# Kernel tuning notes

Measured on AMD Instinct MI355X. Metric: run time of the kernel, lower is better.

## Reference

```python
import jax, jax.numpy as jnp
import numpy as np

PATCH = 64      # patch generator patch size
LD = 1.0        # self.ld
WS = 11         # SSIM gaussian window size
SIGMA = 1.5
C1 = 0.01 ** 2
C2 = 0.03 ** 2


def _gauss_window(channels):
    x = jnp.arange(WS, dtype=jnp.float32)
    g = jnp.exp(-((x - WS // 2) ** 2) / (2.0 * SIGMA * SIGMA))
    g = g / g.sum()
    w2 = jnp.outer(g, g)               # (WS, WS), sums to 1
    return jnp.broadcast_to(w2[None, None], (channels, 1, WS, WS))


def _dwconv(x, w, channels):
    # depthwise 'same' conv, padding = WS//2 (matches F.conv2d(..., padding=ws//2, groups=C))
    p = WS // 2
    return jax.lax.conv_general_dilated(
        x, w, window_strides=(1, 1), padding=[(p, p), (p, p)],
        dimension_numbers=("NCHW", "OIHW", "NCHW"), feature_group_count=channels)


def _ssim(img1, img2):
    # img1, img2: (n, C, h, w) -> per-image mean SSIM, shape (n,)
    ch = img1.shape[1]
    w = _gauss_window(ch).astype(img1.dtype)
    mu1 = _dwconv(img1, w, ch)
    mu2 = _dwconv(img2, w, ch)
    mu1_sq, mu2_sq, mu1_mu2 = mu1 * mu1, mu2 * mu2, mu1 * mu2
    sigma1_sq = _dwconv(img1 * img1, w, ch) - mu1_sq
    sigma2_sq = _dwconv(img2 * img2, w, ch) - mu2_sq
    sigma12 = _dwconv(img1 * img2, w, ch) - mu1_mu2
    ssim_map = ((2.0 * mu1_mu2 + C1) * (2.0 * sigma12 + C2)) / (
        (mu1_sq + mu2_sq + C1) * (sigma1_sq + sigma2_sq + C2))
    return jnp.mean(ssim_map, axis=(1, 2, 3))


def _to_patches(x, ps):
    # (B, C, H, W) -> (B, P, C, ps, ps) with P = (H//ps)*(W//ps)
    B, C, H, W = x.shape
    x = x.reshape(B, C, H // ps, ps, W // ps, ps)
    x = x.transpose(0, 2, 4, 1, 3, 5)
    return x.reshape(B, (H // ps) * (W // ps), C, ps, ps)


def setup_inputs() -> dict:
    key = jax.random.key(0)
    ks = jax.random.split(key, 5)
    shp = (32, 3, 512, 512)
    names = ["A", "N", "GT", "G", "BG"]
    return {n: jax.random.uniform(k, shp, dtype=jnp.float32) for n, k in zip(names, ks)}


def reference(A, N, GT, G, BG):
    pA = _to_patches(A, PATCH)
    pN = _to_patches(N, PATCH)
    pGT = _to_patches(GT, PATCH)
    pG = _to_patches(G, PATCH)
    pBG = _to_patches(BG, PATCH)
    B, P, C, h, w = pA.shape
    # batched SSIM over all (B*P) patches (replaces the python double loop)
    ssim_scores = _ssim(pN.reshape(B * P, C, h, w), pGT.reshape(B * P, C, h, w)).reshape(B, P)
    diff = jnp.minimum(LD * (1.0 - ssim_scores), jnp.ones_like(ssim_scores))
    bg_loss = jnp.mean((pBG - pG) ** 2, axis=(2, 3, 4))
    a_loss = jnp.mean((pA - pG) ** 2, axis=(2, 3, 4))
    loss = diff * bg_loss + (1.0 - diff) * a_loss
    return jnp.sum(loss)
```

## Files before the change

kernel.cpp:

```cpp
#include <hip/hip_runtime.h>
#include <math.h>

#define C1C 1e-4f
#define C2C 9e-4f

#define GW0 0.00102838f
#define GW1 0.00759876f
#define GW2 0.03600077f
#define GW3 0.10936069f
#define GW4 0.21300554f
#define GW5 0.26601173f
__device__ __forceinline__ float conv11(const float* w) {
    float a = GW0 * (w[0] + w[10]);
    a = fmaf(GW1, w[1] + w[9], a);
    a = fmaf(GW2, w[2] + w[8], a);
    a = fmaf(GW3, w[3] + w[7], a);
    a = fmaf(GW4, w[4] + w[6], a);
    a = fmaf(GW5, w[5], a);
    return a;
}

#define SROWS 74
#define SSTR  36

__global__ __launch_bounds__(256, 3) void ssim_fused_kernel(
    const float* __restrict__ A,  const float* __restrict__ Nimg,
    const float* __restrict__ GT, const float* __restrict__ G,
    const float* __restrict__ BG,
    float* __restrict__ ssim_sum, float* __restrict__ sa_sum,
    float* __restrict__ sbg_sum)
{
    __shared__ float S0[SROWS][SSTR];
    __shared__ float S1[SROWS][SSTR];
    __shared__ float S2[SROWS][SSTR];
    __shared__ float S3[SROWS][SSTR];
    __shared__ float S4[SROWS][SSTR];

    const int q  = blockIdx.x;
    const int c  = blockIdx.y;
    const int b  = q >> 6;
    const int pp = q & 63;
    const int ph = pp >> 3;
    const int pw = pp & 7;
    const unsigned base = ((unsigned)(b * 3 + c) << 18)
                        + ((unsigned)(ph * 64) << 9)
                        + (unsigned)(pw * 64);
    const int t = threadIdx.x;

    for (int i = t; i < 10 * SSTR; i += 256) {
        const int r  = i / SSTR;
        const int cc = i - r * SSTR;
        const int rr = (r < 5) ? r : 64 + r;
        S0[rr][cc] = 0.f; S1[rr][cc] = 0.f; S2[rr][cc] = 0.f;
        S3[rr][cc] = 0.f; S4[rr][cc] = 0.f;
    }

    const int hr   = t >> 2;
    const int hseg = t & 3;
    const int c0   = hseg << 3;
    const unsigned rowBase = base + ((unsigned)hr << 9);
    const int vcol = t & 31;
    const int vr0  = (t >> 5) << 3;

    float accS = 0.f;

    for (int h = 0; h < 2; ++h) {
        const int g0 = (h << 5) + c0;
        float xs[18], ys[18];
        #pragma unroll
        for (int m = 0; m < 6; ++m) {
            const int cb = g0 - 8 + 4 * m;
            float4 xv = make_float4(0.f, 0.f, 0.f, 0.f);
            float4 yv = make_float4(0.f, 0.f, 0.f, 0.f);
            if (cb >= 0 && cb < 64) {
                xv = *(const float4*)(Nimg + rowBase + cb);
                yv = *(const float4*)(GT   + rowBase + cb);
            }
            #pragma unroll
            for (int u = 0; u < 4; ++u) {
                const int j = 4 * m + u - 3;
                if (j >= 0 && j < 18) {
                    xs[j] = (&xv.x)[u];
                    ys[j] = (&yv.x)[u];
                }
            }
        }

        {
            float p[18];
            #pragma unroll
            for (int i = 0; i < 18; ++i) p[i] = xs[i] * ys[i];
            #pragma unroll
            for (int mm = 0; mm < 2; ++mm) {
                float4 o;
                #pragma unroll
                for (int u = 0; u < 4; ++u) (&o.x)[u] = conv11(&p[4*mm + u]);
                *(float4*)&S2[5 + hr][c0 + 4*mm] = o;
            }
            #pragma unroll
            for (int i = 0; i < 18; ++i) p[i] = xs[i] * xs[i];
            #pragma unroll
            for (int mm = 0; mm < 2; ++mm) {
                float4 o;
                #pragma unroll
                for (int u = 0; u < 4; ++u) (&o.x)[u] = conv11(&p[4*mm + u]);
                *(float4*)&S0[5 + hr][c0 + 4*mm] = o;
            }
            #pragma unroll
            for (int i = 0; i < 18; ++i) p[i] = ys[i] * ys[i];
            #pragma unroll
            for (int mm = 0; mm < 2; ++mm) {
                float4 o;
                #pragma unroll
                for (int u = 0; u < 4; ++u) (&o.x)[u] = conv11(&p[4*mm + u]);
                *(float4*)&S1[5 + hr][c0 + 4*mm] = o;
            }
            #pragma unroll
            for (int mm = 0; mm < 2; ++mm) {
                float4 o0, o1;
                #pragma unroll
                for (int u = 0; u < 4; ++u) {
                    (&o0.x)[u] = conv11(&xs[4*mm + u]);
                    (&o1.x)[u] = conv11(&ys[4*mm + u]);
                }
                *(float4*)&S3[5 + hr][c0 + 4*mm] = o0;
                *(float4*)&S4[5 + hr][c0 + 4*mm] = o1;
            }
        }
        __syncthreads();

        {
            float Exx[8], Eyy[8], Exy[8], mu1[8];
            float w[18];
            #pragma unroll
            for (int d = 0; d < 18; ++d) w[d] = S0[vr0 + d][vcol];
            #pragma unroll
            for (int o = 0; o < 8; ++o) Exx[o] = conv11(&w[o]);
            #pragma unroll
            for (int d = 0; d < 18; ++d) w[d] = S1[vr0 + d][vcol];
            #pragma unroll
            for (int o = 0; o < 8; ++o) Eyy[o] = conv11(&w[o]);
            #pragma unroll
            for (int d = 0; d < 18; ++d) w[d] = S2[vr0 + d][vcol];
            #pragma unroll
            for (int o = 0; o < 8; ++o) Exy[o] = conv11(&w[o]);
            #pragma unroll
            for (int d = 0; d < 18; ++d) w[d] = S3[vr0 + d][vcol];
            #pragma unroll
            for (int o = 0; o < 8; ++o) mu1[o] = conv11(&w[o]);
            #pragma unroll
            for (int d = 0; d < 18; ++d) w[d] = S4[vr0 + d][vcol];
            #pragma unroll
            for (int o = 0; o < 8; ++o) {
                const float m2  = conv11(&w[o]);
                const float m1  = mu1[o];
                const float m1s = m1 * m1, m2s = m2 * m2, m12 = m1 * m2;
                const float s1  = Exx[o] - m1s;
                const float s2v = Eyy[o] - m2s;
                const float s12 = Exy[o] - m12;
                const float num = (2.f * m12 + C1C) * (2.f * s12 + C2C);
                const float den = (m1s + m2s + C1C) * (s1 + s2v + C2C);
                accS += num / den;
            }
        }
        __syncthreads();
    }

    float sa = 0.f, sbg = 0.f;
    #pragma unroll
    for (int it = 0; it < 4; ++it) {
        const int idx  = t + 256 * it;
        const int row  = idx >> 4;
        const int col4 = (idx & 15) << 2;
        const unsigned off = base + ((unsigned)row << 9) + col4;
        const float4 av  = *(const float4*)(A  + off);
        const float4 gv  = *(const float4*)(G  + off);
        const float4 bgv = *(const float4*)(BG + off);
        float d0 = bgv.x - gv.x, d1 = bgv.y - gv.y, d2 = bgv.z - gv.z, d3 = bgv.w - gv.w;
        sbg += d0*d0 + d1*d1 + d2*d2 + d3*d3;
        float e0 = av.x - gv.x, e1 = av.y - gv.y, e2 = av.z - gv.z, e3 = av.w - gv.w;
        sa  += e0*e0 + e1*e1 + e2*e2 + e3*e3;
    }

    #pragma unroll
    for (int off = 32; off; off >>= 1) {
        accS += __shfl_down(accS, off, 64);
        sa   += __shfl_down(sa,   off, 64);
        sbg  += __shfl_down(sbg,  off, 64);
    }
    const int wv = t >> 6;
    if ((t & 63) == 0) {
        S0[0][wv] = accS; S0[1][wv] = sa; S0[2][wv] = sbg;
    }
    __syncthreads();
    if (t == 0) {
        const int plane = q * 3 + c;
        ssim_sum[plane] = S0[0][0] + S0[0][1] + S0[0][2] + S0[0][3];
        sa_sum[plane]   = S0[1][0] + S0[1][1] + S0[1][2] + S0[1][3];
        sbg_sum[plane]  = S0[2][0] + S0[2][1] + S0[2][2] + S0[2][3];
    }
}

__global__ __launch_bounds__(256) void combine_kernel(
    const float* __restrict__ ssim_sum, const float* __restrict__ sa_sum,
    const float* __restrict__ sbg_sum, float* __restrict__ out)
{
    __shared__ float red[4];
    const int t = threadIdx.x;
    const float invN = 1.f / 12288.f;
    float acc = 0.f;
    #pragma unroll
    for (int r = 0; r < 8; ++r) {
        const int qq = t + 256 * r;
        const float ss = ssim_sum[3*qq] + ssim_sum[3*qq+1] + ssim_sum[3*qq+2];
        const float sa = sa_sum[3*qq]   + sa_sum[3*qq+1]   + sa_sum[3*qq+2];
        const float sb = sbg_sum[3*qq]  + sbg_sum[3*qq+1]  + sbg_sum[3*qq+2];
        const float ssim = ss * invN;
        const float diff = fminf(1.f - ssim, 1.f);
        acc += diff * (sb * invN) + (1.f - diff) * (sa * invN);
    }
    #pragma unroll
    for (int off = 32; off; off >>= 1) acc += __shfl_down(acc, off, 64);
    if ((t & 63) == 0) red[t >> 6] = acc;
    __syncthreads();
    if (t == 0) out[0] = red[0] + red[1] + red[2] + red[3];
}

extern "C" void kernel_launch(void* const* d_in, const int* in_sizes, int n_in,
                              void* d_out, int out_size, void* d_ws, size_t ws_size,
                              hipStream_t stream) {
    const float* A  = (const float*)d_in[0];
    const float* Nn = (const float*)d_in[1];
    const float* GT = (const float*)d_in[2];
    const float* G  = (const float*)d_in[3];
    const float* BG = (const float*)d_in[4];
    float* out      = (float*)d_out;

    float* ssim_sum = (float*)d_ws;
    float* sa_sum   = ssim_sum + 6144;
    float* sbg_sum  = ssim_sum + 12288;

    ssim_fused_kernel<<<dim3(2048, 3), 256, 0, stream>>>(
        A, Nn, GT, G, BG, ssim_sum, sa_sum, sbg_sum);
    combine_kernel<<<1, 256, 0, stream>>>(ssim_sum, sa_sum, sbg_sum, out);
}
```

Measured before the change: 444.6 us.

## Reformulate SSIM statistics via sum/difference images to drop one filtered map

Rewrites the SSIM moments in terms of s=x+y and d=x-y, so only four blurred maps (s, d, s², d²) are needed instead of five (x, y, x², y², xy). This cuts one horizontal and one vertical 11-tap pass plus one shared-memory tile, which lowers LDS footprint and may allow higher occupancy. The final division is also replaced by a hardware reciprocal approximation. This trades a small amount of floating-point accuracy, from cancellation in the variance terms and from the approximate rcp, for fewer arithmetic and LDS operations.

```diff
diff --git a/kernel.cpp b/kernel.cpp
--- a/kernel.cpp
+++ b/kernel.cpp
@@ -34,7 +34,6 @@
     __shared__ float S1[SROWS][SSTR];
     __shared__ float S2[SROWS][SSTR];
     __shared__ float S3[SROWS][SSTR];
-    __shared__ float S4[SROWS][SSTR];
 
     const int q  = blockIdx.x;
     const int c  = blockIdx.y;
@@ -51,8 +50,8 @@
         const int r  = i / SSTR;
         const int cc = i - r * SSTR;
         const int rr = (r < 5) ? r : 64 + r;
-        S0[rr][cc] = 0.f; S1[rr][cc] = 0.f; S2[rr][cc] = 0.f;
-        S3[rr][cc] = 0.f; S4[rr][cc] = 0.f;
+        S0[rr][cc] = 0.f; S1[rr][cc] = 0.f;
+        S2[rr][cc] = 0.f; S3[rr][cc] = 0.f;
     }
 
     const int hr   = t >> 2;
@@ -66,7 +65,7 @@
 
     for (int h = 0; h < 2; ++h) {
         const int g0 = (h << 5) + c0;
-        float xs[18], ys[18];
+        float s[18], d[18];
         #pragma unroll
         for (int m = 0; m < 6; ++m) {
             const int cb = g0 - 8 + 4 * m;
@@ -80,8 +79,8 @@
             for (int u = 0; u < 4; ++u) {
                 const int j = 4 * m + u - 3;
                 if (j >= 0 && j < 18) {
-                    xs[j] = (&xv.x)[u];
-                    ys[j] = (&yv.x)[u];
+                    s[j] = (&xv.x)[u] + (&yv.x)[u];
+                    d[j] = (&xv.x)[u] - (&yv.x)[u];
                 }
             }
         }
@@ -89,16 +88,7 @@
         {
             float p[18];
             #pragma unroll
-            for (int i = 0; i < 18; ++i) p[i] = xs[i] * ys[i];
-            #pragma unroll
-            for (int mm = 0; mm < 2; ++mm) {
-                float4 o;
-                #pragma unroll
-                for (int u = 0; u < 4; ++u) (&o.x)[u] = conv11(&p[4*mm + u]);
-                *(float4*)&S2[5 + hr][c0 + 4*mm] = o;
-            }
-            #pragma unroll
-            for (int i = 0; i < 18; ++i) p[i] = xs[i] * xs[i];
+            for (int i = 0; i < 18; ++i) p[i] = s[i] * s[i];
             #pragma unroll
             for (int mm = 0; mm < 2; ++mm) {
                 float4 o;
@@ -107,7 +97,7 @@
                 *(float4*)&S0[5 + hr][c0 + 4*mm] = o;
             }
             #pragma unroll
-            for (int i = 0; i < 18; ++i) p[i] = ys[i] * ys[i];
+            for (int i = 0; i < 18; ++i) p[i] = d[i] * d[i];
             #pragma unroll
             for (int mm = 0; mm < 2; ++mm) {
                 float4 o;
@@ -120,47 +110,44 @@
                 float4 o0, o1;
                 #pragma unroll
                 for (int u = 0; u < 4; ++u) {
-                    (&o0.x)[u] = conv11(&xs[4*mm + u]);
-                    (&o1.x)[u] = conv11(&ys[4*mm + u]);
+                    (&o0.x)[u] = conv11(&s[4*mm + u]);
+                    (&o1.x)[u] = conv11(&d[4*mm + u]);
                 }
-                *(float4*)&S3[5 + hr][c0 + 4*mm] = o0;
-                *(float4*)&S4[5 + hr][c0 + 4*mm] = o1;
+                *(float4*)&S2[5 + hr][c0 + 4*mm] = o0;
+                *(float4*)&S3[5 + hr][c0 + 4*mm] = o1;
             }
         }
         __syncthreads();
 
         {
-            float Exx[8], Eyy[8], Exy[8], mu1[8];
+            float av[8], bv[8], uv[8];
             float w[18];
             #pragma unroll
-            for (int d = 0; d < 18; ++d) w[d] = S0[vr0 + d][vcol];
-            #pragma unroll
-            for (int o = 0; o < 8; ++o) Exx[o] = conv11(&w[o]);
-            #pragma unroll
-            for (int d = 0; d < 18; ++d) w[d] = S1[vr0 + d][vcol];
-            #pragma unroll
-            for (int o = 0; o < 8; ++o) Eyy[o] = conv11(&w[o]);
-            #pragma unroll
-            for (int d = 0; d < 18; ++d) w[d] = S2[vr0 + d][vcol];
-            #pragma unroll
-            for (int o = 0; o < 8; ++o) Exy[o] = conv11(&w[o]);
-            #pragma unroll
-            for (int d = 0; d < 18; ++d) w[d] = S3[vr0 + d][vcol];
-            #pragma unroll
-            for (int o = 0; o < 8; ++o) mu1[o] = conv11(&w[o]);
-            #pragma unroll
-            for (int d = 0; d < 18; ++d) w[d] = S4[vr0 + d][vcol];
+            for (int dd = 0; dd < 18; ++dd) w[dd] = S2[vr0 + dd][vcol];
+            #pragma unroll
+            for (int o = 0; o < 8; ++o) av[o] = conv11(&w[o]);
+            #pragma unroll
+            for (int dd = 0; dd < 18; ++dd) w[dd] = S3[vr0 + dd][vcol];
+            #pragma unroll
+            for (int o = 0; o < 8; ++o) bv[o] = conv11(&w[o]);
+            #pragma unroll
+            for (int dd = 0; dd < 18; ++dd) w[dd] = S0[vr0 + dd][vcol];
+            #pragma unroll
+            for (int o = 0; o < 8; ++o) uv[o] = conv11(&w[o]);
+            #pragma unroll
+            for (int dd = 0; dd < 18; ++dd) w[dd] = S1[vr0 + dd][vcol];
             #pragma unroll
             for (int o = 0; o < 8; ++o) {
-                const float m2  = conv11(&w[o]);
-                const float m1  = mu1[o];
-                const float m1s = m1 * m1, m2s = m2 * m2, m12 = m1 * m2;
-                const float s1  = Exx[o] - m1s;
-                const float s2v = Eyy[o] - m2s;
-                const float s12 = Exy[o] - m12;
-                const float num = (2.f * m12 + C1C) * (2.f * s12 + C2C);
-                const float den = (m1s + m2s + C1C) * (s1 + s2v + C2C);
-                accS += num / den;
+                const float vvv = conv11(&w[o]);
+                const float A2  = av[o] * av[o];
+                const float B2  = bv[o] * bv[o];
+                const float twoM12 = 0.5f * (A2 - B2);
+                const float sumSq  = 0.5f * (A2 + B2);
+                const float numL = twoM12 + C1C;
+                const float denL = sumSq  + C1C;
+                const float numR = fmaf(0.5f, uv[o] - vvv, C2C - twoM12);
+                const float denR = fmaf(0.5f, uv[o] + vvv, C2C - sumSq);
+                accS += (numL * numR) * __builtin_amdgcn_rcpf(denL * denR);
             }
         }
         __syncthreads();
```

New measurement: 440.0 us. No clear change (-1.0%).
